# Performance work log

Hardware: AMD Instinct MI355X
Metric: run time of the kernel (lower is better)

## Reference

```python
import jax, jax.numpy as jnp
import numpy as np

TAU = 2.0
V_THRESHOLD = 1.0
ALPHA = 4.0  # surrogate gradient sharpness


@jax.custom_vjp
def heaviside_sg(x):
    # torch.heaviside(x, 1.0): 1 for x >= 0, 0 for x < 0
    return (x >= 0).astype(x.dtype)


def _heaviside_sg_fwd(x):
    return heaviside_sg(x), x


def _heaviside_sg_bwd(x, g):
    sg = jax.nn.sigmoid(ALPHA * x)
    return (g * (1.0 - sg) * sg * ALPHA,)


heaviside_sg.defvjp(_heaviside_sg_fwd, _heaviside_sg_bwd)


def setup_inputs() -> dict:
    key = jax.random.key(0)
    T, B, C, H, W = 32, 32, 128, 32, 32
    x = jax.random.normal(key, (T, B, C, H, W), dtype=jnp.float32)
    return {"x": x}


def reference(x):
    # x: [T, B, C, H, W]; LIF scan over time with carry v
    def step(v, x_t):
        v = v + (x_t - v) / TAU                      # leaky integrate
        spike = heaviside_sg(v - V_THRESHOLD)         # fire (surrogate grad)
        v = (1.0 - jax.lax.stop_gradient(spike)) * v  # hard reset (detached)
        return v, spike

    v0 = jnp.zeros_like(x[0])
    _, spikes = jax.lax.scan(step, v0, x)
    return spikes
```

## Files before the change

kernel.cpp:

```cpp
#include <hip/hip_runtime.h>


__global__ __launch_bounds__(256) void lif_fwd_kernel(
    const float4* __restrict__ x, float4* __restrict__ out,
    int n4, int T) {
  int n = blockIdx.x * blockDim.x + threadIdx.x;
  if (n >= n4) return;

  float vx = 0.0f, vy = 0.0f, vz = 0.0f, vw = 0.0f;

  for (int t = 0; t < T; ++t) {
    float4 xt = x[(size_t)t * n4 + n];

    vx = vx + (xt.x - vx) * 0.5f;
    vy = vy + (xt.y - vy) * 0.5f;
    vz = vz + (xt.z - vz) * 0.5f;
    vw = vw + (xt.w - vw) * 0.5f;

    float4 s;
    s.x = (vx - 1.0f >= 0.0f) ? 1.0f : 0.0f;
    s.y = (vy - 1.0f >= 0.0f) ? 1.0f : 0.0f;
    s.z = (vz - 1.0f >= 0.0f) ? 1.0f : 0.0f;
    s.w = (vw - 1.0f >= 0.0f) ? 1.0f : 0.0f;

    vx = (1.0f - s.x) * vx;
    vy = (1.0f - s.y) * vy;
    vz = (1.0f - s.z) * vz;
    vw = (1.0f - s.w) * vw;

    out[(size_t)t * n4 + n] = s;
  }
}

extern "C" void kernel_launch(void* const* d_in, const int* in_sizes, int n_in,
                              void* d_out, int out_size, void* d_ws, size_t ws_size,
                              hipStream_t stream) {
  const float* x = (const float*)d_in[0];
  float* out = (float*)d_out;

  const int T = 32;
  const int total = in_sizes[0];
  const int N = total / T;
  const int n4 = N / 4;

  const int block = 256;
  const int grid = (n4 + block - 1) / block;

  lif_fwd_kernel<<<grid, block, 0, stream>>>(
      (const float4*)x, (float4*)out, n4, T);
}
```

Measured before the change: 218.6 us.

## Process two float4 columns per thread with prefetch and nontemporal loads/stores

Each thread now handles two float4 columns 256 apart, halving the grid. The next timestep's input is loaded one iteration ahead so loads overlap compute, and all loads and stores use nontemporal hints to avoid polluting cache on a pure streaming workload. The bounds check is removed, which assumes n4 is divisible by 512.

```diff
diff --git a/kernel.cpp b/kernel.cpp
--- a/kernel.cpp
+++ b/kernel.cpp
@@ -1,34 +1,62 @@
 #include <hip/hip_runtime.h>
 
 
+typedef float f32x4 __attribute__((ext_vector_type(4)));
+
+__device__ __forceinline__ f32x4 lif_step(f32x4& v, const f32x4 xt) {
+  f32x4 s;
+  v.x = v.x + (xt.x - v.x) * 0.5f;
+  v.y = v.y + (xt.y - v.y) * 0.5f;
+  v.z = v.z + (xt.z - v.z) * 0.5f;
+  v.w = v.w + (xt.w - v.w) * 0.5f;
+  s.x = (v.x - 1.0f >= 0.0f) ? 1.0f : 0.0f;
+  s.y = (v.y - 1.0f >= 0.0f) ? 1.0f : 0.0f;
+  s.z = (v.z - 1.0f >= 0.0f) ? 1.0f : 0.0f;
+  s.w = (v.w - 1.0f >= 0.0f) ? 1.0f : 0.0f;
+  v.x *= (1.0f - s.x);
+  v.y *= (1.0f - s.y);
+  v.z *= (1.0f - s.z);
+  v.w *= (1.0f - s.w);
+  return s;
+}
+
 __global__ __launch_bounds__(256) void lif_fwd_kernel(
-    const float4* __restrict__ x, float4* __restrict__ out,
+    const f32x4* __restrict__ x, f32x4* __restrict__ out,
     int n4, int T) {
-  int n = blockIdx.x * blockDim.x + threadIdx.x;
-  if (n >= n4) return;
+  const int i = blockIdx.x * 512 + threadIdx.x;
 
-  float vx = 0.0f, vy = 0.0f, vz = 0.0f, vw = 0.0f;
+  const f32x4* __restrict__ px = x + i;
+  f32x4* __restrict__ po = out + i;
 
-  for (int t = 0; t < T; ++t) {
-    float4 xt = x[(size_t)t * n4 + n];
+  f32x4 v0 = (f32x4){0.f, 0.f, 0.f, 0.f};
+  f32x4 v1 = (f32x4){0.f, 0.f, 0.f, 0.f};
 
-    vx = vx + (xt.x - vx) * 0.5f;
-    vy = vy + (xt.y - vy) * 0.5f;
-    vz = vz + (xt.z - vz) * 0.5f;
-    vw = vw + (xt.w - vw) * 0.5f;
+  f32x4 a = __builtin_nontemporal_load(px);
+  f32x4 b = __builtin_nontemporal_load(px + 256);
 
-    float4 s;
-    s.x = (vx - 1.0f >= 0.0f) ? 1.0f : 0.0f;
-    s.y = (vy - 1.0f >= 0.0f) ? 1.0f : 0.0f;
-    s.z = (vz - 1.0f >= 0.0f) ? 1.0f : 0.0f;
-    s.w = (vw - 1.0f >= 0.0f) ? 1.0f : 0.0f;
+  #pragma unroll 4
+  for (int t = 0; t < T - 1; ++t) {
+    const size_t offn = (size_t)(t + 1) * n4;
+    f32x4 na = __builtin_nontemporal_load(px + offn);
+    f32x4 nb = __builtin_nontemporal_load(px + offn + 256);
 
-    vx = (1.0f - s.x) * vx;
-    vy = (1.0f - s.y) * vy;
-    vz = (1.0f - s.z) * vz;
-    vw = (1.0f - s.w) * vw;
+    f32x4 s0 = lif_step(v0, a);
+    f32x4 s1 = lif_step(v1, b);
 
-    out[(size_t)t * n4 + n] = s;
+    const size_t offo = (size_t)t * n4;
+    __builtin_nontemporal_store(s0, po + offo);
+    __builtin_nontemporal_store(s1, po + offo + 256);
+
+    a = na;
+    b = nb;
+  }
+
+  {
+    f32x4 s0 = lif_step(v0, a);
+    f32x4 s1 = lif_step(v1, b);
+    const size_t offo = (size_t)(T - 1) * n4;
+    __builtin_nontemporal_store(s0, po + offo);
+    __builtin_nontemporal_store(s1, po + offo + 256);
   }
 }
 
@@ -44,8 +72,8 @@
   const int n4 = N / 4;
 
   const int block = 256;
-  const int grid = (n4 + block - 1) / block;
+  const int grid = n4 / (block * 2);
 
   lif_fwd_kernel<<<grid, block, 0, stream>>>(
-      (const float4*)x, (float4*)out, n4, T);
+      (const f32x4*)x, (f32x4*)out, n4, T);
 }
```

After: 195.2 us. 1.12x faster.
